# Kernel tuning notes

Measured on AMD Instinct MI355X. Metric: run time of the kernel, lower is better.

## Reference

```python
import jax, jax.numpy as jnp
import numpy as np
from jax import lax

D_MODEL = 512
D_STATE = 16
D_CONV = 4
DT_RANK = 32  # ceil(512/16)
BATCH = 4
SEQ = 2048
FN = 32


def setup_inputs() -> dict:
    key = jax.random.key(0)
    ks = jax.random.split(key, 12)
    s = 0.02
    d, n, r = D_MODEL, D_STATE, DT_RANK
    return {
        "atoms": jax.random.normal(ks[0], (BATCH, SEQ, d), jnp.float32),
        # normalized "adjacency"-like matrix so delta_p = dis_dense @ delta stays O(1)
        "dis_dense": jax.random.uniform(ks[1], (BATCH, SEQ, SEQ), jnp.float32) / SEQ,
        "gpt_emb": jax.random.normal(ks[2], (BATCH, d), jnp.float32),
        "fg_emb": jax.random.normal(ks[3], (BATCH, FN, d), jnp.float32),
        "in_proj_w": jax.random.normal(ks[4], (2 * d, d), jnp.float32) * s,
        "conv_w": jax.random.normal(ks[5], (d, 1, D_CONV), jnp.float32) * s,  # depthwise OIW
        "conv_b": jnp.zeros((d,), jnp.float32),
        "x_proj_w": jax.random.normal(ks[6], (r + 2 * n, d), jnp.float32) * s,
        "dt_proj_w": jax.random.normal(ks[7], (d, r), jnp.float32) * s,
        "dt_proj_b": jnp.full((d,), 0.5, jnp.float32),
        "A_log": jnp.log(jnp.broadcast_to(jnp.arange(1, n + 1, dtype=jnp.float32), (d, n))),
        "D_param": jnp.ones((d,), jnp.float32),
        "out_proj_w": jax.random.normal(ks[8], (d, d), jnp.float32) * s,
        "film_w1": jax.random.normal(ks[9], (d, d), jnp.float32) * s,
        "film_b1": jnp.zeros((d,), jnp.float32),
        "film_w2": jax.random.normal(ks[10], (2 * d, d), jnp.float32) * s,
        "film_b2": jnp.zeros((2 * d,), jnp.float32),
    }


def reference(atoms, dis_dense, gpt_emb, fg_emb,
              in_proj_w, conv_w, conv_b, x_proj_w, dt_proj_w, dt_proj_b,
              A_log, D_param, out_proj_w, film_w1, film_b1, film_w2, film_b2):
    b, l, d = atoms.shape
    n = A_log.shape[1]

    # --- CrossAttentionFusion: Q=atoms, K/V=fg_emb ---
    scores = jnp.einsum('bld,bfd->blf', atoms, fg_emb) / (d ** 0.5)
    attn = jax.nn.softmax(scores, axis=-1)
    x = atoms + jnp.einsum('blf,bfd->bld', attn, fg_emb)

    # --- FiLM modulation from gpt_emb ---
    h = jax.nn.silu(gpt_emb @ film_w1.T + film_b1)
    gamma, beta = jnp.split(h @ film_w2.T + film_b2, 2, axis=-1)
    x = x * gamma[:, None, :] + beta[:, None, :]

    # --- in_proj and split into (x, res) ---
    xs, res = jnp.split(x @ in_proj_w.T, 2, axis=-1)

    # --- depthwise causal-padded conv1d, truncate to l ---
    xc = jnp.transpose(xs, (0, 2, 1))  # [b, d, l]
    xc = lax.conv_general_dilated(xc, conv_w, window_strides=(1,),
                                  padding=[(D_CONV - 1, D_CONV - 1)],
                                  feature_group_count=d)[:, :, :l]
    xc = xc + conv_b[None, :, None]
    u = jax.nn.silu(jnp.transpose(xc, (0, 2, 1)))  # [b, l, d]

    # --- SSM ---
    A = -jnp.exp(A_log)                      # [d, n]
    x_dbl = u @ x_proj_w.T                   # [b, l, r+2n]
    delta, Bm, Cm = jnp.split(x_dbl, [DT_RANK, DT_RANK + n], axis=-1)
    delta = jax.nn.softplus(delta @ dt_proj_w.T + dt_proj_b)  # [b, l, d]
    delta_p = jnp.einsum('blk,bkd->bld', dis_dense, delta)     # graph-mixed delta

    deltaA = jnp.exp(delta_p[..., None] * A)                   # [b, l, d, n]
    deltaB_u = delta_p[..., None] * Bm[:, :, None, :] * u[..., None]  # [b, l, d, n]

    def step(carry, inp):
        dA_t, dBu_t, C_t = inp
        carry = dA_t * carry + dBu_t                # [b, d, n]
        y_t = jnp.einsum('bdn,bn->bd', carry, C_t)
        return carry, y_t

    init = jnp.zeros((b, d, n), deltaA.dtype)
    _, ys = lax.scan(step, init,
                     (jnp.moveaxis(deltaA, 1, 0),
                      jnp.moveaxis(deltaB_u, 1, 0),
                      jnp.moveaxis(Cm, 1, 0)))
    y = jnp.moveaxis(ys, 0, 1) + u * D_param       # [b, l, d]

    # --- gate, out_proj, nonfinite -> 0 ---
    y = y * jax.nn.silu(res)
    out = y @ out_proj_w.T
    return jnp.where(jnp.isfinite(out), out, 0.0)
```

## Files before the change

### kernel.cpp

```cpp
#include <hip/hip_runtime.h>
#include <stdint.h>

#define D_MODEL 512
#define D_STATE 16
#define DT_RANK 32
#define SEQ 2048
#define NBATCH 4
#define FN 32
#define CHUNK 16
#define NCHUNK 128
#define DPPLANE ((size_t)8192*D_MODEL)

typedef unsigned short u16;
using s16x8 = __attribute__((ext_vector_type(8))) short;
using f32x4 = __attribute__((ext_vector_type(4))) float;
using f32x8 = __attribute__((ext_vector_type(8))) float;
using bf16x8 = __attribute__((ext_vector_type(8))) __bf16;

typedef __attribute__((address_space(3))) void lds_void;
typedef __attribute__((address_space(1))) const void glb_void;

__device__ __forceinline__ void gload16(const void* g, void* l) {
  __builtin_amdgcn_global_load_lds((glb_void*)g, (lds_void*)l, 16, 0, 0);
}

__device__ inline u16 f2bf(float f) {
  uint32_t u = __float_as_uint(f);
  u += 0x7FFFu + ((u >> 16) & 1u);
  return (u16)(u >> 16);
}
__device__ __forceinline__ float bf2f(u16 v) {
  return __uint_as_float((uint32_t)v << 16);
}

__device__ __forceinline__ s16x8 pack8bf(float4 lo, float4 hi) {
  f32x8 v;
  v[0] = lo.x; v[1] = lo.y; v[2] = lo.z; v[3] = lo.w;
  v[4] = hi.x; v[5] = hi.y; v[6] = hi.z; v[7] = hi.w;
  bf16x8 b = __builtin_convertvector(v, bf16x8);
  return __builtin_bit_cast(s16x8, b);
}

__global__ __launch_bounds__(256) void film1_kernel(
    const float* __restrict__ gpt, const float* __restrict__ w1,
    const float* __restrict__ b1, float* __restrict__ h)
{
  int b = blockIdx.y, r0 = blockIdx.x*16, t = threadIdx.x;
  __shared__ float g[D_MODEL];
  for (int i = t; i < D_MODEL; i += 256) g[i] = gpt[b*D_MODEL + i];
  __syncthreads();
  int r = r0 + (t >> 4), ln = t & 15;
  const float* wr = &w1[(size_t)r*D_MODEL + ln*32];
  const float* gg = &g[ln*32];
  float s = 0.f;
  #pragma unroll
  for (int k = 0; k < 32; k += 4) {
    float4 w = *(const float4*)&wr[k];
    s += w.x*gg[k] + w.y*gg[k+1] + w.z*gg[k+2] + w.w*gg[k+3];
  }
  s += __shfl_down(s, 8); s += __shfl_down(s, 4);
  s += __shfl_down(s, 2); s += __shfl_down(s, 1);
  if (ln == 0) { float v = s + b1[r]; h[b*D_MODEL + r] = v / (1.f + expf(-v)); }
}

__global__ __launch_bounds__(256) void film2_kernel(
    const float* __restrict__ h, const float* __restrict__ w2,
    const float* __restrict__ b2, float* __restrict__ gb)
{
  int b = blockIdx.y, r0 = blockIdx.x*16, t = threadIdx.x;
  __shared__ float hs[D_MODEL];
  for (int i = t; i < D_MODEL; i += 256) hs[i] = h[b*D_MODEL + i];
  __syncthreads();
  int r = r0 + (t >> 4), ln = t & 15;
  const float* wr = &w2[(size_t)r*D_MODEL + ln*32];
  const float* gg = &hs[ln*32];
  float s = 0.f;
  #pragma unroll
  for (int k = 0; k < 32; k += 4) {
    float4 w = *(const float4*)&wr[k];
    s += w.x*gg[k] + w.y*gg[k+1] + w.z*gg[k+2] + w.w*gg[k+3];
  }
  s += __shfl_down(s, 8); s += __shfl_down(s, 4);
  s += __shfl_down(s, 2); s += __shfl_down(s, 1);
  if (ln == 0) gb[b*1024 + r] = s + b2[r];
}

__global__ __launch_bounds__(256) void build_fgpad_kernel(
    const float* __restrict__ fg, u16* __restrict__ fgpad)
{
  int row = blockIdx.x & 127, b = blockIdx.x >> 7, t = threadIdx.x;
  u16* dst = &fgpad[((size_t)b*128 + row)*D_MODEL];
  if (row < FN) {
    const float* src = &fg[((size_t)b*FN + row)*D_MODEL];
    float2 v = *(const float2*)&src[t*2];
    dst[t*2] = f2bf(v.x); dst[t*2+1] = f2bf(v.y);
  } else {
    dst[t*2] = 0; dst[t*2+1] = 0;
  }
}

__global__ __launch_bounds__(256) void pv_film_kernel(
    const float* __restrict__ atoms, const float* __restrict__ fg,
    const float* __restrict__ scores, const float* __restrict__ gb,
    u16* __restrict__ xout)
{
  int wave = threadIdx.x >> 6, lane = threadIdx.x & 63;
  int row = blockIdx.x*4 + wave;
  int b = row >> 11;
  float s = scores[(size_t)row*128 + (lane & 31)] * 0.04419417382415922f;
  float m = s;
  #pragma unroll
  for (int o = 16; o; o >>= 1) m = fmaxf(m, __shfl_xor(m, o));
  float e = __expf(s - m);
  float sum = e;
  #pragma unroll
  for (int o = 16; o; o >>= 1) sum += __shfl_xor(sum, o);
  float my_attn = e / sum;

  int d0 = lane*8;
  const float* arow = &atoms[(size_t)row*D_MODEL + d0];
  float4 acc0 = *(const float4*)&arow[0];
  float4 acc1 = *(const float4*)&arow[4];
  const float* fgb = &fg[(size_t)b*FN*D_MODEL + d0];
  #pragma unroll 8
  for (int f = 0; f < FN; f++) {
    float w = __shfl(my_attn, f);
    float4 g0 = *(const float4*)&fgb[(size_t)f*D_MODEL];
    float4 g1 = *(const float4*)&fgb[(size_t)f*D_MODEL + 4];
    acc0.x += w*g0.x; acc0.y += w*g0.y; acc0.z += w*g0.z; acc0.w += w*g0.w;
    acc1.x += w*g1.x; acc1.y += w*g1.y; acc1.z += w*g1.z; acc1.w += w*g1.w;
  }
  const float* gbg = &gb[(size_t)b*1024 + d0];
  float4 gm0 = *(const float4*)&gbg[0];
  float4 gm1 = *(const float4*)&gbg[4];
  float4 bt0 = *(const float4*)&gbg[D_MODEL];
  float4 bt1 = *(const float4*)&gbg[D_MODEL + 4];
  s16x8 o;
  o[0] = (short)f2bf(acc0.x*gm0.x + bt0.x);
  o[1] = (short)f2bf(acc0.y*gm0.y + bt0.y);
  o[2] = (short)f2bf(acc0.z*gm0.z + bt0.z);
  o[3] = (short)f2bf(acc0.w*gm0.w + bt0.w);
  o[4] = (short)f2bf(acc1.x*gm1.x + bt1.x);
  o[5] = (short)f2bf(acc1.y*gm1.y + bt1.y);
  o[6] = (short)f2bf(acc1.z*gm1.z + bt1.z);
  o[7] = (short)f2bf(acc1.w*gm1.w + bt1.w);
  *(s16x8*)&xout[(size_t)row*D_MODEL + d0] = o;
}

__global__ __launch_bounds__(256) void cvt_bf16_kernel(
    const float* __restrict__ in, u16* __restrict__ out, int n4)
{
  int i = blockIdx.x*256 + threadIdx.x;
  if (i >= n4) return;
  float4 v = *(const float4*)&in[(size_t)i*4];
  ushort4 o; o.x = f2bf(v.x); o.y = f2bf(v.y); o.z = f2bf(v.z); o.w = f2bf(v.w);
  *(ushort4*)&out[(size_t)i*4] = o;
}

__global__ __launch_bounds__(256) void build_wcomb_kernel(
    const float* __restrict__ dtw, const float* __restrict__ xpw, u16* __restrict__ w)
{
  int row = blockIdx.x, t = threadIdx.x;
  if (row < D_MODEL) {
    __shared__ float dr[DT_RANK];
    if (t < DT_RANK) dr[t] = dtw[row*DT_RANK + t];
    __syncthreads();
    for (int k = t; k < D_MODEL; k += 256) {
      float s = 0.f;
      #pragma unroll
      for (int r = 0; r < DT_RANK; r++) s += dr[r] * xpw[r*D_MODEL + k];
      w[(size_t)row*D_MODEL + k] = f2bf(s);
    }
  } else if (row < D_MODEL + 32) {
    for (int k = t; k < D_MODEL; k += 256)
      w[(size_t)row*D_MODEL + k] = f2bf(xpw[(size_t)(DT_RANK + row - D_MODEL)*D_MODEL + k]);
  } else {
    for (int k = t; k < D_MODEL; k += 256)
      w[(size_t)row*D_MODEL + k] = 0;
  }
}

__global__ __launch_bounds__(256) void gemm_bt64_kernel(
    const u16* __restrict__ A, const u16* __restrict__ B, float* __restrict__ C,
    int M, int N, int K, int clampFinite)
{
  int gx = gridDim.x, gy = gridDim.y;
  int flat = blockIdx.x + gx*blockIdx.y;
  int cpx = (gx*gy) >> 3;
  flat = (flat & 7)*cpx + (flat >> 3);
  int bx = flat % gx, by = flat / gx;
  int m0 = by * 64, n0 = bx * 128;
  __shared__ u16 As[2][64][32];
  __shared__ u16 Bs[2][128][32];
  int tid = threadIdx.x, lane = tid & 63, wave = tid >> 6;
  int wm = (wave >> 1) * 32, wn = (wave & 1) * 64;
  int fr = lane & 15, fk = (lane >> 4) * 8;
  int srow = tid >> 2, scol = (tid & 3) * 8;
  const u16* abase  = &A[(size_t)(m0 + srow)*K + scol];
  const u16* b0base = &B[(size_t)(n0 + srow)*K + scol];
  const u16* b1base = &B[(size_t)(n0 + 64 + srow)*K + scol];
  gload16(abase,  &As[0][srow][scol]);
  gload16(b0base, &Bs[0][srow][scol]);
  gload16(b1base, &Bs[0][64 + srow][scol]);
  __syncthreads();
  f32x4 acc[2][4] = {};
  int NT = K >> 5, cur = 0;
  for (int t = 0; t < NT; t++) {
    int nxt = cur ^ 1;
    if (t + 1 < NT) {
      int k0 = (t + 1) << 5;
      gload16(&abase[k0],  &As[nxt][srow][scol]);
      gload16(&b0base[k0], &Bs[nxt][srow][scol]);
      gload16(&b1base[k0], &Bs[nxt][64 + srow][scol]);
    }
    s16x8 af[2], bf[4];
    #pragma unroll
    for (int i = 0; i < 2; i++) af[i] = *(const s16x8*)(&As[cur][wm + i*16 + fr][fk]);
    #pragma unroll
    for (int i = 0; i < 4; i++) bf[i] = *(const s16x8*)(&Bs[cur][wn + i*16 + fr][fk]);
    #pragma unroll
    for (int mi = 0; mi < 2; mi++)
      #pragma unroll
      for (int ni = 0; ni < 4; ni++)
        acc[mi][ni] = __builtin_amdgcn_mfma_f32_16x16x32_bf16(af[mi], bf[ni], acc[mi][ni], 0, 0, 0);
    __syncthreads();
    cur = nxt;
  }
  int cr = (lane >> 4) * 4, cc = lane & 15;
  #pragma unroll
  for (int mi = 0; mi < 2; mi++)
    #pragma unroll
    for (int ni = 0; ni < 4; ni++) {
      int rowb = m0 + wm + mi*16 + cr, col = n0 + wn + ni*16 + cc;
      #pragma unroll
      for (int r = 0; r < 4; r++) {
        float v = acc[mi][ni][r];
        if (clampFinite && !isfinite(v)) v = 0.f;
        C[(size_t)(rowb + r)*N + col] = v;
      }
    }
}

__global__ __launch_bounds__(256) void gemm_f32a_kernel(
    const float* __restrict__ Ag, const u16* __restrict__ Bg, float* __restrict__ Cg,
    int M, int N, int K, long long azs, long long bzs, long long czs,
    int clampFinite, int swz)
{
  int gx = gridDim.x, gy = gridDim.y;
  int flat = blockIdx.x + gx*(blockIdx.y + gy*blockIdx.z);
  if (swz) {
    int cpx = (gx*gy*(int)gridDim.z) >> 3;
    flat = (flat & 7)*cpx + (flat >> 3);
  }
  int bx = flat % gx, tmp = flat / gx;
  int by = tmp % gy, bz = tmp / gy;
  const float* A = Ag + (size_t)bz * azs;
  const u16* B = Bg + (size_t)bz * bzs;
  float* C = Cg + (size_t)bz * czs;
  int m0 = by * 128, n0 = bx * 128;
  __shared__ u16 As[128][32];
  __shared__ u16 Bs[128][32];
  int tid = threadIdx.x, lane = tid & 63, wave = tid >> 6;
  int wm = (wave >> 1) * 64, wn = (wave & 1) * 64;
  int fr = lane & 15, fk = (lane >> 4) * 8;
  int srow = tid >> 2, scol = (tid & 3) * 8;
  f32x4 acc[4][4] = {};
  for (int k0 = 0; k0 < K; k0 += 32) {
    const float* a0p = &A[(size_t)(m0 + srow)*K + k0 + scol];
    const float* a1p = &A[(size_t)(m0 + 64 + srow)*K + k0 + scol];
    float4 a00 = *(const float4*)&a0p[0];
    float4 a01 = *(const float4*)&a0p[4];
    float4 a10 = *(const float4*)&a1p[0];
    float4 a11 = *(const float4*)&a1p[4];
    gload16(&B[(size_t)(n0 + srow)*K + k0 + scol],      &Bs[srow][scol]);
    gload16(&B[(size_t)(n0 + 64 + srow)*K + k0 + scol], &Bs[64 + srow][scol]);
    *(s16x8*)&As[srow][scol]      = pack8bf(a00, a01);
    *(s16x8*)&As[64 + srow][scol] = pack8bf(a10, a11);
    __syncthreads();
    s16x8 af[4], bf[4];
    #pragma unroll
    for (int i = 0; i < 4; i++) af[i] = *(const s16x8*)(&As[wm + i*16 + fr][fk]);
    #pragma unroll
    for (int i = 0; i < 4; i++) bf[i] = *(const s16x8*)(&Bs[wn + i*16 + fr][fk]);
    #pragma unroll
    for (int mi = 0; mi < 4; mi++)
      #pragma unroll
      for (int ni = 0; ni < 4; ni++)
        acc[mi][ni] = __builtin_amdgcn_mfma_f32_16x16x32_bf16(af[mi], bf[ni], acc[mi][ni], 0, 0, 0);
    __syncthreads();
  }
  int cr = (lane >> 4) * 4, cc = lane & 15;
  #pragma unroll
  for (int mi = 0; mi < 4; mi++)
    #pragma unroll
    for (int ni = 0; ni < 4; ni++) {
      int rowb = m0 + wm + mi*16 + cr, col = n0 + wn + ni*16 + cc;
      #pragma unroll
      for (int r = 0; r < 4; r++) {
        float v = acc[mi][ni][r];
        if (clampFinite && !isfinite(v)) v = 0.f;
        C[(size_t)(rowb + r)*N + col] = v;
      }
    }
}

__global__ __launch_bounds__(256) void gemm_dpbf_splitk_kernel(
    const u16* __restrict__ disbf, const u16* __restrict__ deltaT,
    u16* __restrict__ dpp)
{
  int gx = gridDim.x, gy = gridDim.y;
  int flat = blockIdx.x + gx*(blockIdx.y + gy*blockIdx.z);
  int cpx = (gx*gy*(int)gridDim.z) >> 3;
  flat = (flat & 7)*cpx + (flat >> 3);
  int bx = flat % gx, tmp = flat / gx;
  int by = tmp % gy, bz = tmp / gy;
  int b = bz >> 2, ks = bz & 3;
  const u16* A = disbf  + (size_t)b*SEQ*SEQ     + ks*512;
  const u16* B = deltaT + (size_t)b*D_MODEL*SEQ + ks*512;
  u16*       C = dpp    + (size_t)ks*DPPLANE    + (size_t)b*SEQ*D_MODEL;
  int m0 = by * 128, n0 = bx * 128;
  __shared__ u16 As[128][32];
  __shared__ u16 Bs[128][32];
  int tid = threadIdx.x, lane = tid & 63, wave = tid >> 6;
  int wm = (wave >> 1) * 64, wn = (wave & 1) * 64;
  int fr = lane & 15, fk = (lane >> 4) * 8;
  int srow = tid >> 2, scol = (tid & 3) * 8;
  f32x4 acc[4][4] = {};
  for (int k0 = 0; k0 < 512; k0 += 32) {
    gload16(&A[(size_t)(m0 + srow)*SEQ + k0 + scol],      &As[srow][scol]);
    gload16(&A[(size_t)(m0 + 64 + srow)*SEQ + k0 + scol], &As[64 + srow][scol]);
    gload16(&B[(size_t)(n0 + srow)*SEQ + k0 + scol],      &Bs[srow][scol]);
    gload16(&B[(size_t)(n0 + 64 + srow)*SEQ + k0 + scol], &Bs[64 + srow][scol]);
    __syncthreads();
    s16x8 af[4], bf[4];
    #pragma unroll
    for (int i = 0; i < 4; i++) af[i] = *(const s16x8*)(&As[wm + i*16 + fr][fk]);
    #pragma unroll
    for (int i = 0; i < 4; i++) bf[i] = *(const s16x8*)(&Bs[wn + i*16 + fr][fk]);
    #pragma unroll
    for (int mi = 0; mi < 4; mi++)
      #pragma unroll
      for (int ni = 0; ni < 4; ni++)
        acc[mi][ni] = __builtin_amdgcn_mfma_f32_16x16x32_bf16(af[mi], bf[ni], acc[mi][ni], 0, 0, 0);
    __syncthreads();
  }
  int cr = (lane >> 4) * 4, cc = lane & 15;
  #pragma unroll
  for (int mi = 0; mi < 4; mi++)
    #pragma unroll
    for (int ni = 0; ni < 4; ni++) {
      int rowb = m0 + wm + mi*16 + cr, col = n0 + wn + ni*16 + cc;
      #pragma unroll
      for (int r = 0; r < 4; r++)
        C[(size_t)(rowb + r)*D_MODEL + col] = f2bf(acc[mi][ni][r]);
    }
}

__global__ __launch_bounds__(256) void gemm_delta_kernel(
    const u16* __restrict__ A, const u16* __restrict__ B,
    const float* __restrict__ dtb, u16* __restrict__ deltaT,
    float* __restrict__ Bv, float* __restrict__ Cv)
{
  int gx = gridDim.x, gy = gridDim.y;
  int flat = blockIdx.x + gx*blockIdx.y;
  int cpx = (gx*gy) >> 3;
  flat = (flat & 7)*cpx + (flat >> 3);
  int bx = flat % gx, by = flat / gx;
  int m0 = by * 64, n0 = bx * 128;
  __shared__ u16 As[64][32];
  __shared__ u16 Bs[128][32];
  int tid = threadIdx.x, lane = tid & 63, wave = tid >> 6;
  int wm = (wave >> 1) * 32, wn = (wave & 1) * 64;
  int fr = lane & 15, fk = (lane >> 4) * 8;
  int srow = tid >> 2, scol = (tid & 3) * 8;
  f32x4 acc[2][4] = {};
  for (int k0 = 0; k0 < D_MODEL; k0 += 32) {
    gload16(&A[(size_t)(m0 + srow)*D_MODEL + k0 + scol],      &As[srow][scol]);
    gload16(&B[(size_t)(n0 + srow)*D_MODEL + k0 + scol],      &Bs[srow][scol]);
    gload16(&B[(size_t)(n0 + 64 + srow)*D_MODEL + k0 + scol], &Bs[64 + srow][scol]);
    __syncthreads();
    s16x8 af[2], bf[4];
    #pragma unroll
    for (int i = 0; i < 2; i++) af[i] = *(const s16x8*)(&As[wm + i*16 + fr][fk]);
    #pragma unroll
    for (int i = 0; i < 4; i++) bf[i] = *(const s16x8*)(&Bs[wn + i*16 + fr][fk]);
    #pragma unroll
    for (int mi = 0; mi < 2; mi++)
      #pragma unroll
      for (int ni = 0; ni < 4; ni++)
        acc[mi][ni] = __builtin_amdgcn_mfma_f32_16x16x32_bf16(af[mi], bf[ni], acc[mi][ni], 0, 0, 0);
    __syncthreads();
  }
  int cr = (lane >> 4) * 4, cc = lane & 15;
  #pragma unroll
  for (int mi = 0; mi < 2; mi++)
    #pragma unroll
    for (int ni = 0; ni < 4; ni++) {
      int rowb = m0 + wm + mi*16 + cr, col = n0 + wn + ni*16 + cc;
      if (col < D_MODEL) {
        float bias = dtb[col];
        #pragma unroll
        for (int r = 0; r < 4; r++) {
          float v = acc[mi][ni][r] + bias;
          v = (v > 20.f) ? v : log1pf(expf(v));
          int gr = rowb + r;
          deltaT[((size_t)(gr >> 11)*D_MODEL + col)*SEQ + (gr & (SEQ-1))] = f2bf(v);
        }
      } else if (col < D_MODEL + 16) {
        #pragma unroll
        for (int r = 0; r < 4; r++)
          Bv[(size_t)(rowb + r)*D_STATE + (col - D_MODEL)] = acc[mi][ni][r];
      } else if (col < D_MODEL + 32) {
        #pragma unroll
        for (int r = 0; r < 4; r++)
          Cv[(size_t)(rowb + r)*D_STATE + (col - D_MODEL - 16)] = acc[mi][ni][r];
      }
    }
}

__global__ __launch_bounds__(256) void conv_silu_kernel(
    const float* __restrict__ xsres, const float* __restrict__ cw,
    const float* __restrict__ cb, float* __restrict__ u, u16* __restrict__ ubf)
{
  int idx = blockIdx.x*256 + threadIdx.x;
  int d = (idx & 127) * 4;
  int row = idx >> 7;
  int l = row & (SEQ - 1);
  float w[4][4];
  #pragma unroll
  for (int c = 0; c < 4; c++) *(float4*)w[c] = *(const float4*)&cw[(d + c)*4];
  float4 acc = *(const float4*)&cb[d];
  #pragma unroll
  for (int k = 0; k < 4; k++) {
    int li = l - 3 + k;
    if (li >= 0) {
      float4 v = *(const float4*)&xsres[(size_t)(row - 3 + k)*1024 + d];
      acc.x += v.x*w[0][k]; acc.y += v.y*w[1][k];
      acc.z += v.z*w[2][k]; acc.w += v.w*w[3][k];
    }
  }
  float4 o;
  o.x = acc.x/(1.f+expf(-acc.x)); o.y = acc.y/(1.f+expf(-acc.y));
  o.z = acc.z/(1.f+expf(-acc.z)); o.w = acc.w/(1.f+expf(-acc.w));
  *(float4*)&u[(size_t)row*D_MODEL + d] = o;
  ushort4 ob;
  ob.x = f2bf(o.x); ob.y = f2bf(o.y); ob.z = f2bf(o.z); ob.w = f2bf(o.w);
  *(ushort4*)&ubf[(size_t)row*D_MODEL + d] = ob;
}

__global__ __launch_bounds__(256) void scanA_kernel(
    const u16* __restrict__ dpp, const float* __restrict__ u,
    const float* __restrict__ Bv, const float* __restrict__ A_log,
    float* __restrict__ dpf, float* __restrict__ slocal, float* __restrict__ sumdp_out)
{
  int d = blockIdx.x*256 + threadIdx.x;
  int c = blockIdx.y, b = blockIdx.z;
  __shared__ float Bs[CHUNK][D_STATE];
  int t = threadIdx.x;
  size_t lbase = (size_t)b*SEQ + c*CHUNK;
  Bs[t >> 4][t & 15] = Bv[(lbase + (t >> 4))*D_STATE + (t & 15)];
  float a[D_STATE];
  #pragma unroll
  for (int n = 0; n < D_STATE; n += 4) {
    float4 v = *(const float4*)&A_log[(size_t)d*D_STATE + n];
    a[n] = -expf(v.x); a[n+1] = -expf(v.y); a[n+2] = -expf(v.z); a[n+3] = -expf(v.w);
  }
  __syncthreads();
  float s[D_STATE];
  #pragma unroll
  for (int n = 0; n < D_STATE; n++) s[n] = 0.f;
  float sd = 0.f;
  for (int j = 0; j < CHUNK; j++) {
    size_t r = lbase + j;
    size_t idx = r*D_MODEL + d;
    float dpv = bf2f(dpp[idx]) + bf2f(dpp[idx + DPPLANE])
              + bf2f(dpp[idx + 2*DPPLANE]) + bf2f(dpp[idx + 3*DPPLANE]);
    dpf[idx] = dpv;
    float uv  = u[idx];
    sd += dpv;
    float dbu = dpv * uv;
    #pragma unroll
    for (int n = 0; n < D_STATE; n++)
      s[n] = __expf(a[n]*dpv)*s[n] + dbu*Bs[j][n];
  }
  size_t obase = ((size_t)b*NCHUNK + c)*D_MODEL + d;
  #pragma unroll
  for (int n = 0; n < D_STATE; n += 4)
    *(float4*)&slocal[obase*D_STATE + n] = make_float4(s[n], s[n+1], s[n+2], s[n+3]);
  sumdp_out[obase] = sd;
}

__global__ __launch_bounds__(256) void scanB_kernel(
    const float* __restrict__ slocal, const float* __restrict__ sumdp,
    const float* __restrict__ A_log, float* __restrict__ sIn)
{
  int g = blockIdx.x*256 + threadIdx.x;
  int n = g & 15, d = (g >> 4) & (D_MODEL - 1), b = g >> 13;
  float a = -expf(A_log[d*D_STATE + n]);
  float s = 0.f;
  for (int c = 0; c < NCHUNK; c++) {
    size_t idx = ((size_t)b*NCHUNK + c)*D_MODEL + d;
    sIn[idx*D_STATE + n] = s;
    s = __expf(a * sumdp[idx]) * s + slocal[idx*D_STATE + n];
  }
}

__global__ __launch_bounds__(256) void scanC_kernel(
    const float* __restrict__ dp, const float* __restrict__ u,
    const float* __restrict__ Bv, const float* __restrict__ Cv,
    const float* __restrict__ A_log, const float* __restrict__ Dp,
    const float* __restrict__ xsres, const float* __restrict__ sIn,
    u16* __restrict__ yout)
{
  int d = blockIdx.x*256 + threadIdx.x;
  int c = blockIdx.y, b = blockIdx.z;
  __shared__ float Bs[CHUNK][D_STATE];
  __shared__ float Cs[CHUNK][D_STATE];
  int t = threadIdx.x;
  size_t lbase = (size_t)b*SEQ + c*CHUNK;
  Bs[t >> 4][t & 15] = Bv[(lbase + (t >> 4))*D_STATE + (t & 15)];
  Cs[t >> 4][t & 15] = Cv[(lbase + (t >> 4))*D_STATE + (t & 15)];
  float a[D_STATE];
  #pragma unroll
  for (int n = 0; n < D_STATE; n += 4) {
    float4 v = *(const float4*)&A_log[(size_t)d*D_STATE + n];
    a[n] = -expf(v.x); a[n+1] = -expf(v.y); a[n+2] = -expf(v.z); a[n+3] = -expf(v.w);
  }
  float s[D_STATE];
  size_t ibase = (((size_t)b*NCHUNK + c)*D_MODEL + d)*D_STATE;
  #pragma unroll
  for (int n = 0; n < D_STATE; n += 4) {
    float4 v = *(const float4*)&sIn[ibase + n];
    s[n] = v.x; s[n+1] = v.y; s[n+2] = v.z; s[n+3] = v.w;
  }
  float dparam = Dp[d];
  __syncthreads();
  for (int j = 0; j < CHUNK; j++) {
    size_t r = lbase + j;
    float dpv = dp[r*D_MODEL + d];
    float uv  = u[r*D_MODEL + d];
    float dbu = dpv * uv;
    float y = 0.f;
    #pragma unroll
    for (int n = 0; n < D_STATE; n++) {
      s[n] = __expf(a[n]*dpv)*s[n] + dbu*Bs[j][n];
      y += s[n]*Cs[j][n];
    }
    y += uv * dparam;
    float rr = xsres[r*1024 + D_MODEL + d];
    y *= rr/(1.f + __expf(-rr));
    yout[r*D_MODEL + d] = f2bf(y);
  }
}

extern "C" void kernel_launch(void* const* d_in, const int* in_sizes, int n_in,
                              void* d_out, int out_size, void* d_ws, size_t ws_size,
                              hipStream_t stream)
{
  const float* atoms  = (const float*)d_in[0];
  const float* dis    = (const float*)d_in[1];
  const float* gpt    = (const float*)d_in[2];
  const float* fg     = (const float*)d_in[3];
  const float* inw    = (const float*)d_in[4];
  const float* convw  = (const float*)d_in[5];
  const float* convb  = (const float*)d_in[6];
  const float* xpw    = (const float*)d_in[7];
  const float* dtw    = (const float*)d_in[8];
  const float* dtb    = (const float*)d_in[9];
  const float* A_log  = (const float*)d_in[10];
  const float* Dparam = (const float*)d_in[11];
  const float* outw   = (const float*)d_in[12];
  const float* fw1    = (const float*)d_in[13];
  const float* fb1    = (const float*)d_in[14];
  const float* fw2    = (const float*)d_in[15];
  const float* fb2    = (const float*)d_in[16];

  char* ws = (char*)d_ws;
  size_t off = 0;
  auto alloc = [&](size_t bytes) { char* p = ws + off; off += (bytes + 255) & ~255ull; return p; };
  float* gb     = (float*)alloc((size_t)NBATCH*1024*4);
  float* hbuf   = (float*)alloc((size_t)NBATCH*512*4);
  u16*   fgpad  = (u16*)  alloc((size_t)NBATCH*128*512*2);
  float* scores = (float*)alloc((size_t)NBATCH*2048*128*4);
  u16*   xbf    = (u16*)  alloc((size_t)8192*512*2);
  u16*   inwbf  = (u16*)  alloc((size_t)1024*512*2);
  u16*   outwbf = (u16*)  alloc((size_t)512*512*2);
  u16*   wcomb  = (u16*)  alloc((size_t)640*512*2);
  float* xsres  = (float*)alloc((size_t)8192*1024*4);
  u16*   dpp    = (u16*)  alloc(4*DPPLANE*2);
  float* dpf    = (float*)alloc(DPPLANE*4);
  float* ubuf   = (float*)alloc((size_t)8192*512*4);
  u16*   ubf    = (u16*)  alloc((size_t)8192*512*2);
  float* Bv     = (float*)alloc((size_t)8192*16*4);
  float* Cv     = (float*)alloc((size_t)8192*16*4);
  u16*   deltaT = (u16*)  alloc((size_t)NBATCH*512*2048*2);
  float* slocal = (float*)alloc((size_t)NBATCH*NCHUNK*512*16*4);
  float* sumdp  = (float*)alloc((size_t)NBATCH*NCHUNK*512*4);
  float* sIn    = (float*)alloc((size_t)NBATCH*NCHUNK*512*16*4);
  u16*   disbf  = (u16*)slocal;

  film1_kernel<<<dim3(32, NBATCH), 256, 0, stream>>>(gpt, fw1, fb1, hbuf);
  film2_kernel<<<dim3(64, NBATCH), 256, 0, stream>>>(hbuf, fw2, fb2, gb);

  build_fgpad_kernel<<<NBATCH*128, 256, 0, stream>>>(fg, fgpad);
  gemm_f32a_kernel<<<dim3(1, 2048/128, NBATCH), 256, 0, stream>>>(
      atoms, fgpad, scores, 2048, 128, 512,
      (long long)2048*512, (long long)128*512, (long long)2048*128, 0, 1);
  pv_film_kernel<<<8192/4, 256, 0, stream>>>(atoms, fg, scores, gb, xbf);

  cvt_bf16_kernel<<<(1024*512/4)/256, 256, 0, stream>>>(inw, inwbf, 1024*512/4);
  cvt_bf16_kernel<<<(512*512/4)/256, 256, 0, stream>>>(outw, outwbf, 512*512/4);
  cvt_bf16_kernel<<<(NBATCH*2048*2048/4)/256, 256, 0, stream>>>(dis, disbf, NBATCH*2048*2048/4);
  build_wcomb_kernel<<<640, 256, 0, stream>>>(dtw, xpw, wcomb);

  gemm_bt64_kernel<<<dim3(1024/128, 8192/64), 256, 0, stream>>>(
      xbf, inwbf, xsres, 8192, 1024, 512, 0);
  conv_silu_kernel<<<8192*128/256, 256, 0, stream>>>(xsres, convw, convb, ubuf, ubf);

  gemm_delta_kernel<<<dim3(640/128, 8192/64), 256, 0, stream>>>(
      ubf, wcomb, dtb, deltaT, Bv, Cv);

  gemm_dpbf_splitk_kernel<<<dim3(512/128, 2048/128, NBATCH*4), 256, 0, stream>>>(
      disbf, deltaT, dpp);

  scanA_kernel<<<dim3(2, NCHUNK, NBATCH), 256, 0, stream>>>(dpp, ubuf, Bv, A_log, dpf, slocal, sumdp);
  scanB_kernel<<<32768/256, 256, 0, stream>>>(slocal, sumdp, A_log, sIn);
  u16* ybf = xbf;
  scanC_kernel<<<dim3(2, NCHUNK, NBATCH), 256, 0, stream>>>(dpf, ubuf, Bv, Cv, A_log, Dparam, xsres, sIn, ybf);

  gemm_bt64_kernel<<<dim3(512/128, 8192/64), 256, 0, stream>>>(
      ybf, outwbf, (float*)d_out, 8192, 512, 512, 1);
}
```

Baseline: 250.2 us.

## Store in_proj output and u in bf16, drop fp32 u buffer, merge prep kernels

The in_proj GEMM gains a bf16 output mode, so the xsres intermediate (8192x1024) is stored as bf16 instead of fp32. The fp32 copy of u is dropped, and conv, scanA and scanC read the bf16 buffers instead. Four small weight-conversion and padding launches are merged into one prep kernel. This halves traffic on the large intermediates and saves launch overhead, at the cost of bf16 rounding on the u and res values feeding the scan and gate.

After: 237.5 us. -5.0%, faster.

```diff
diff --git a/kernel.cpp b/kernel.cpp
--- a/kernel.cpp
+++ b/kernel.cpp
@@ -85,17 +85,53 @@
   if (ln == 0) gb[b*1024 + r] = s + b2[r];
 }
 
-__global__ __launch_bounds__(256) void build_fgpad_kernel(
-    const float* __restrict__ fg, u16* __restrict__ fgpad)
-{
-  int row = blockIdx.x & 127, b = blockIdx.x >> 7, t = threadIdx.x;
-  u16* dst = &fgpad[((size_t)b*128 + row)*D_MODEL];
-  if (row < FN) {
-    const float* src = &fg[((size_t)b*FN + row)*D_MODEL];
-    float2 v = *(const float2*)&src[t*2];
-    dst[t*2] = f2bf(v.x); dst[t*2+1] = f2bf(v.y);
+__global__ __launch_bounds__(256) void prep_kernel(
+    const float* __restrict__ fg, const float* __restrict__ inw,
+    const float* __restrict__ outw, const float* __restrict__ dtw,
+    const float* __restrict__ xpw,
+    u16* __restrict__ fgpad, u16* __restrict__ inwbf,
+    u16* __restrict__ outwbf, u16* __restrict__ wcomb)
+{
+  int blk = blockIdx.x, t = threadIdx.x;
+  if (blk < 512) {
+    int row = blk & 127, b = blk >> 7;
+    u16* dst = &fgpad[((size_t)b*128 + row)*D_MODEL];
+    if (row < FN) {
+      const float* src = &fg[((size_t)b*FN + row)*D_MODEL];
+      float2 v = *(const float2*)&src[t*2];
+      dst[t*2] = f2bf(v.x); dst[t*2+1] = f2bf(v.y);
+    } else {
+      dst[t*2] = 0; dst[t*2+1] = 0;
+    }
+  } else if (blk < 1536) {
+    int row = blk - 512;
+    float2 v = *(const float2*)&inw[(size_t)row*D_MODEL + t*2];
+    inwbf[(size_t)row*D_MODEL + t*2]     = f2bf(v.x);
+    inwbf[(size_t)row*D_MODEL + t*2 + 1] = f2bf(v.y);
+  } else if (blk < 2048) {
+    int row = blk - 1536;
+    float2 v = *(const float2*)&outw[(size_t)row*D_MODEL + t*2];
+    outwbf[(size_t)row*D_MODEL + t*2]     = f2bf(v.x);
+    outwbf[(size_t)row*D_MODEL + t*2 + 1] = f2bf(v.y);
   } else {
-    dst[t*2] = 0; dst[t*2+1] = 0;
+    int row = blk - 2048;
+    if (row < D_MODEL) {
+      __shared__ float dr[DT_RANK];
+      if (t < DT_RANK) dr[t] = dtw[row*DT_RANK + t];
+      __syncthreads();
+      for (int k = t; k < D_MODEL; k += 256) {
+        float s = 0.f;
+        #pragma unroll
+        for (int r = 0; r < DT_RANK; r++) s += dr[r] * xpw[r*D_MODEL + k];
+        wcomb[(size_t)row*D_MODEL + k] = f2bf(s);
+      }
+    } else if (row < D_MODEL + 32) {
+      for (int k = t; k < D_MODEL; k += 256)
+        wcomb[(size_t)row*D_MODEL + k] = f2bf(xpw[(size_t)(DT_RANK + row - D_MODEL)*D_MODEL + k]);
+    } else {
+      for (int k = t; k < D_MODEL; k += 256)
+        wcomb[(size_t)row*D_MODEL + k] = 0;
+    }
   }
 }
 
@@ -157,32 +193,9 @@
   *(ushort4*)&out[(size_t)i*4] = o;
 }
 
-__global__ __launch_bounds__(256) void build_wcomb_kernel(
-    const float* __restrict__ dtw, const float* __restrict__ xpw, u16* __restrict__ w)
-{
-  int row = blockIdx.x, t = threadIdx.x;
-  if (row < D_MODEL) {
-    __shared__ float dr[DT_RANK];
-    if (t < DT_RANK) dr[t] = dtw[row*DT_RANK + t];
-    __syncthreads();
-    for (int k = t; k < D_MODEL; k += 256) {
-      float s = 0.f;
-      #pragma unroll
-      for (int r = 0; r < DT_RANK; r++) s += dr[r] * xpw[r*D_MODEL + k];
-      w[(size_t)row*D_MODEL + k] = f2bf(s);
-    }
-  } else if (row < D_MODEL + 32) {
-    for (int k = t; k < D_MODEL; k += 256)
-      w[(size_t)row*D_MODEL + k] = f2bf(xpw[(size_t)(DT_RANK + row - D_MODEL)*D_MODEL + k]);
-  } else {
-    for (int k = t; k < D_MODEL; k += 256)
-      w[(size_t)row*D_MODEL + k] = 0;
-  }
-}
-
 __global__ __launch_bounds__(256) void gemm_bt64_kernel(
-    const u16* __restrict__ A, const u16* __restrict__ B, float* __restrict__ C,
-    int M, int N, int K, int clampFinite)
+    const u16* __restrict__ A, const u16* __restrict__ B, void* __restrict__ Cv_,
+    int M, int N, int K, int outMode)
 {
   int gx = gridDim.x, gy = gridDim.y;
   int flat = blockIdx.x + gx*blockIdx.y;
@@ -227,18 +240,32 @@
     cur = nxt;
   }
   int cr = (lane >> 4) * 4, cc = lane & 15;
-  #pragma unroll
-  for (int mi = 0; mi < 2; mi++)
-    #pragma unroll
-    for (int ni = 0; ni < 4; ni++) {
-      int rowb = m0 + wm + mi*16 + cr, col = n0 + wn + ni*16 + cc;
-      #pragma unroll
-      for (int r = 0; r < 4; r++) {
-        float v = acc[mi][ni][r];
-        if (clampFinite && !isfinite(v)) v = 0.f;
-        C[(size_t)(rowb + r)*N + col] = v;
+  if (outMode == 2) {
+    u16* C = (u16*)Cv_;
+    #pragma unroll
+    for (int mi = 0; mi < 2; mi++)
+      #pragma unroll
+      for (int ni = 0; ni < 4; ni++) {
+        int rowb = m0 + wm + mi*16 + cr, col = n0 + wn + ni*16 + cc;
+        #pragma unroll
+        for (int r = 0; r < 4; r++)
+          C[(size_t)(rowb + r)*N + col] = f2bf(acc[mi][ni][r]);
       }
-    }
+  } else {
+    float* C = (float*)Cv_;
+    #pragma unroll
+    for (int mi = 0; mi < 2; mi++)
+      #pragma unroll
+      for (int ni = 0; ni < 4; ni++) {
+        int rowb = m0 + wm + mi*16 + cr, col = n0 + wn + ni*16 + cc;
+        #pragma unroll
+        for (int r = 0; r < 4; r++) {
+          float v = acc[mi][ni][r];
+          if (outMode == 1 && !isfinite(v)) v = 0.f;
+          C[(size_t)(rowb + r)*N + col] = v;
+        }
+      }
+  }
 }
 
 __global__ __launch_bounds__(256) void gemm_f32a_kernel(
@@ -419,8 +446,8 @@
 }
 
 __global__ __launch_bounds__(256) void conv_silu_kernel(
-    const float* __restrict__ xsres, const float* __restrict__ cw,
-    const float* __restrict__ cb, float* __restrict__ u, u16* __restrict__ ubf)
+    const u16* __restrict__ xsres, const float* __restrict__ cw,
+    const float* __restrict__ cb, u16* __restrict__ ubf)
 {
   int idx = blockIdx.x*256 + threadIdx.x;
   int d = (idx & 127) * 4;
@@ -434,22 +461,21 @@
   for (int k = 0; k < 4; k++) {
     int li = l - 3 + k;
     if (li >= 0) {
-      float4 v = *(const float4*)&xsres[(size_t)(row - 3 + k)*1024 + d];
-      acc.x += v.x*w[0][k]; acc.y += v.y*w[1][k];
-      acc.z += v.z*w[2][k]; acc.w += v.w*w[3][k];
+      ushort4 v = *(const ushort4*)&xsres[(size_t)(row - 3 + k)*1024 + d];
+      acc.x += bf2f(v.x)*w[0][k]; acc.y += bf2f(v.y)*w[1][k];
+      acc.z += bf2f(v.z)*w[2][k]; acc.w += bf2f(v.w)*w[3][k];
     }
   }
   float4 o;
   o.x = acc.x/(1.f+expf(-acc.x)); o.y = acc.y/(1.f+expf(-acc.y));
   o.z = acc.z/(1.f+expf(-acc.z)); o.w = acc.w/(1.f+expf(-acc.w));
-  *(float4*)&u[(size_t)row*D_MODEL + d] = o;
   ushort4 ob;
   ob.x = f2bf(o.x); ob.y = f2bf(o.y); ob.z = f2bf(o.z); ob.w = f2bf(o.w);
   *(ushort4*)&ubf[(size_t)row*D_MODEL + d] = ob;
 }
 
 __global__ __launch_bounds__(256) void scanA_kernel(
-    const u16* __restrict__ dpp, const float* __restrict__ u,
+    const u16* __restrict__ dpp, const u16* __restrict__ ubf,
     const float* __restrict__ Bv, const float* __restrict__ A_log,
     float* __restrict__ dpf, float* __restrict__ slocal, float* __restrict__ sumdp_out)
 {
@@ -476,7 +502,7 @@
     float dpv = bf2f(dpp[idx]) + bf2f(dpp[idx + DPPLANE])
               + bf2f(dpp[idx + 2*DPPLANE]) + bf2f(dpp[idx + 3*DPPLANE]);
     dpf[idx] = dpv;
-    float uv  = u[idx];
+    float uv  = bf2f(ubf[idx]);
     sd += dpv;
     float dbu = dpv * uv;
     #pragma unroll
@@ -506,10 +532,10 @@
 }
 
 __global__ __launch_bounds__(256) void scanC_kernel(
-    const float* __restrict__ dp, const float* __restrict__ u,
+    const float* __restrict__ dp, const u16* __restrict__ ubf,
     const float* __restrict__ Bv, const float* __restrict__ Cv,
     const float* __restrict__ A_log, const float* __restrict__ Dp,
-    const float* __restrict__ xsres, const float* __restrict__ sIn,
+    const u16* __restrict__ xsres, const float* __restrict__ sIn,
     u16* __restrict__ yout)
 {
   int d = blockIdx.x*256 + threadIdx.x;
@@ -538,7 +564,7 @@
   for (int j = 0; j < CHUNK; j++) {
     size_t r = lbase + j;
     float dpv = dp[r*D_MODEL + d];
-    float uv  = u[r*D_MODEL + d];
+    float uv  = bf2f(ubf[r*D_MODEL + d]);
     float dbu = dpv * uv;
     float y = 0.f;
     #pragma unroll
@@ -547,7 +573,7 @@
       y += s[n]*Cs[j][n];
     }
     y += uv * dparam;
-    float rr = xsres[r*1024 + D_MODEL + d];
+    float rr = bf2f(xsres[r*1024 + D_MODEL + d]);
     y *= rr/(1.f + __expf(-rr));
     yout[r*D_MODEL + d] = f2bf(y);
   }
@@ -586,10 +612,9 @@
   u16*   inwbf  = (u16*)  alloc((size_t)1024*512*2);
   u16*   outwbf = (u16*)  alloc((size_t)512*512*2);
   u16*   wcomb  = (u16*)  alloc((size_t)640*512*2);
-  float* xsres  = (float*)alloc((size_t)8192*1024*4);
+  u16*   xsres  = (u16*)  alloc((size_t)8192*1024*2);
   u16*   dpp    = (u16*)  alloc(4*DPPLANE*2);
   float* dpf    = (float*)alloc(DPPLANE*4);
-  float* ubuf   = (float*)alloc((size_t)8192*512*4);
   u16*   ubf    = (u16*)  alloc((size_t)8192*512*2);
   float* Bv     = (float*)alloc((size_t)8192*16*4);
   float* Cv     = (float*)alloc((size_t)8192*16*4);
@@ -601,21 +626,17 @@
 
   film1_kernel<<<dim3(32, NBATCH), 256, 0, stream>>>(gpt, fw1, fb1, hbuf);
   film2_kernel<<<dim3(64, NBATCH), 256, 0, stream>>>(hbuf, fw2, fb2, gb);
-
-  build_fgpad_kernel<<<NBATCH*128, 256, 0, stream>>>(fg, fgpad);
+  prep_kernel<<<2688, 256, 0, stream>>>(fg, inw, outw, dtw, xpw, fgpad, inwbf, outwbf, wcomb);
+  cvt_bf16_kernel<<<(NBATCH*2048*2048/4)/256, 256, 0, stream>>>(dis, disbf, NBATCH*2048*2048/4);
+
   gemm_f32a_kernel<<<dim3(1, 2048/128, NBATCH), 256, 0, stream>>>(
       atoms, fgpad, scores, 2048, 128, 512,
       (long long)2048*512, (long long)128*512, (long long)2048*128, 0, 1);
   pv_film_kernel<<<8192/4, 256, 0, stream>>>(atoms, fg, scores, gb, xbf);
 
-  cvt_bf16_kernel<<<(1024*512/4)/256, 256, 0, stream>>>(inw, inwbf, 1024*512/4);
-  cvt_bf16_kernel<<<(512*512/4)/256, 256, 0, stream>>>(outw, outwbf, 512*512/4);
-  cvt_bf16_kernel<<<(NBATCH*2048*2048/4)/256, 256, 0, stream>>>(dis, disbf, NBATCH*2048*2048/4);
-  build_wcomb_kernel<<<640, 256, 0, stream>>>(dtw, xpw, wcomb);
-
   gemm_bt64_kernel<<<dim3(1024/128, 8192/64), 256, 0, stream>>>(
-      xbf, inwbf, xsres, 8192, 1024, 512, 0);
-  conv_silu_kernel<<<8192*128/256, 256, 0, stream>>>(xsres, convw, convb, ubuf, ubf);
+      xbf, inwbf, xsres, 8192, 1024, 512, 2);
+  conv_silu_kernel<<<8192*128/256, 256, 0, stream>>>(xsres, convw, convb, ubf);
 
   gemm_delta_kernel<<<dim3(640/128, 8192/64), 256, 0, stream>>>(
       ubf, wcomb, dtb, deltaT, Bv, Cv);
@@ -623,10 +644,10 @@
   gemm_dpbf_splitk_kernel<<<dim3(512/128, 2048/128, NBATCH*4), 256, 0, stream>>>(
       disbf, deltaT, dpp);
 
-  scanA_kernel<<<dim3(2, NCHUNK, NBATCH), 256, 0, stream>>>(dpp, ubuf, Bv, A_log, dpf, slocal, sumdp);
+  scanA_kernel<<<dim3(2, NCHUNK, NBATCH), 256, 0, stream>>>(dpp, ubf, Bv, A_log, dpf, slocal, sumdp);
   scanB_kernel<<<32768/256, 256, 0, stream>>>(slocal, sumdp, A_log, sIn);
   u16* ybf = xbf;
-  scanC_kernel<<<dim3(2, NCHUNK, NBATCH), 256, 0, stream>>>(dpf, ubuf, Bv, Cv, A_log, Dparam, xsres, sIn, ybf);
+  scanC_kernel<<<dim3(2, NCHUNK, NBATCH), 256, 0, stream>>>(dpf, ubf, Bv, Cv, A_log, Dparam, xsres, sIn, ybf);
 
   gemm_bt64_kernel<<<dim3(512/128, 8192/64), 256, 0, stream>>>(
       ybf, outwbf, (float*)d_out, 8192, 512, 512, 1);
```
